# Optimization experiments

Hardware: AMD Instinct MI355X
Metric: run time of the kernel (lower is better)

The kernel has to match this reference:

```python
import jax, jax.numpy as jnp
import numpy as np

H = 4          # num_attention_heads
DH = 32        # attention_head_size
C = H * DH     # all_head_size = 128
WS = 7         # window side -> dim = 49
DIM = WS * WS
B = 4096       # number of windows
TABLE = (2 * WS - 1) ** 2  # 169


def setup_inputs() -> dict:
    key = jax.random.key(0)
    ks = jax.random.split(key, 10)
    s = 0.02
    return {
        "hidden_states": jax.random.normal(ks[0], (B, DIM, C), jnp.float32),
        "attention_mask": jax.random.normal(ks[1], (B, DIM, DIM), jnp.float32),
        "Wq": jax.random.normal(ks[2], (C, C), jnp.float32) * s,
        "bq": jax.random.normal(ks[3], (C,), jnp.float32) * s,
        "Wk": jax.random.normal(ks[4], (C, C), jnp.float32) * s,
        "bk": jax.random.normal(ks[5], (C,), jnp.float32) * s,
        "Wv": jax.random.normal(ks[6], (C, C), jnp.float32) * s,
        "bv": jax.random.normal(ks[7], (C,), jnp.float32) * s,
        "relative_position_bias_table": jax.random.normal(ks[8], (TABLE, H), jnp.float32) * s,
        "relative_position_index": jax.random.randint(ks[9], (DIM * DIM,), 0, TABLE, jnp.int64),
    }


def reference(hidden_states, attention_mask, Wq, bq, Wk, bk, Wv, bv,
              relative_position_bias_table, relative_position_index):
    b, n, _ = hidden_states.shape
    # QKV projections -> [b, H, n, DH]
    def proj(W, bias):
        y = jnp.einsum('bnc,cd->bnd', hidden_states, W.T) + bias
        return y.reshape(b, n, H, DH).transpose(0, 2, 1, 3)
    q = proj(Wq, bq)
    k = proj(Wk, bk)
    v = proj(Wv, bv)
    scores = jnp.einsum('bhnd,bhmd->bhnm', q, k) / jnp.sqrt(jnp.float32(DH))
    # relative position bias gather: [n*n] -> [n, n, H] -> [H, n, n]
    bias = relative_position_bias_table[relative_position_index].reshape(n, n, H)
    bias = bias.transpose(2, 0, 1)
    scores = scores + bias[None] + attention_mask[:, None]
    probs = jax.nn.softmax(scores, axis=-1)
    ctx = jnp.einsum('bhnm,bhmd->bhnd', probs, v)
    ctx = ctx.transpose(0, 2, 1, 3).reshape(b, n, H * DH)
    return ctx
```

## Files before the change

kernel.cpp:

```cpp
#include <hip/hip_runtime.h>
#include <hip/hip_bf16.h>


#define SEQ 49
#define CH 128
#define NH 4
#define DHD 32
#define NTAB 169

typedef __hip_bfloat16 bf16;
typedef __attribute__((ext_vector_type(8))) short bf16x8;
typedef __attribute__((ext_vector_type(4))) float f32x4;

#define LDQ 136
#define LDP 72
#define PROWS 52
#define OFF_Q  0
#define OFF_K  (64*LDQ)
#define OFF_VT (2*64*LDQ)
#define SMEM_ELEMS (OFF_VT + CH*LDP)
#define SMEM_BYTES (SMEM_ELEMS*2)

__device__ __forceinline__ bf16x8 pack8(float4 a, float4 b) {
    alignas(16) bf16 t[8] = {
        __float2bfloat16(a.x), __float2bfloat16(a.y),
        __float2bfloat16(a.z), __float2bfloat16(a.w),
        __float2bfloat16(b.x), __float2bfloat16(b.y),
        __float2bfloat16(b.z), __float2bfloat16(b.w)};
    return *(const bf16x8*)t;
}

__global__ void bias_precompute_kernel(const float* __restrict__ table,
                                       const int* __restrict__ ridx,
                                       float* __restrict__ bias_pad) {
    int i = blockIdx.x*256 + threadIdx.x;
    if (i >= NH*64*64) return;
    int h = i >> 12, nq = (i >> 6) & 63, mk = i & 63;
    float v = 0.f;
    if (nq < SEQ && mk < SEQ) {
        int idx = ridx[nq*SEQ + mk];
        idx = idx < 0 ? 0 : (idx > NTAB-1 ? NTAB-1 : idx);
        v = table[idx*NH + h];
    }
    bias_pad[i] = v;
}

template<bool USEWS>
__global__ __launch_bounds__(256, 3) void swin_attn_kernel(
    const float* __restrict__ hs,
    const float* __restrict__ amask,
    const float* __restrict__ Wq, const float* __restrict__ bq,
    const float* __restrict__ Wk, const float* __restrict__ bk,
    const float* __restrict__ Wv, const float* __restrict__ bv,
    const float* __restrict__ table,
    const int*  __restrict__ ridx,
    const float* __restrict__ bias_pad,
    float* __restrict__ out)
{
    extern __shared__ bf16 smem[];
    const int tid  = threadIdx.x;
    const int b    = blockIdx.x;
    const int wave = tid >> 6;
    const int lane = tid & 63;
    const int quad = lane >> 4;
    const int l    = lane & 15;

    bf16* sQ  = smem + OFF_Q;
    bf16* sK  = smem + OFF_K;
    bf16* sVt = smem + OFF_VT;
    bf16* sP  = smem;

    bf16x8 aX[4][4];
    const bf16x8 zf = {0,0,0,0,0,0,0,0};
    const float* xb = hs + (size_t)b*SEQ*CH + quad*8;
#pragma unroll
    for (int mt = 0; mt < 4; ++mt) {
        const int row = mt*16 + l;
        if (row < SEQ) {
            const float* xr = xb + row*CH;
#pragma unroll
            for (int ks = 0; ks < 4; ++ks)
                aX[mt][ks] = pack8(*(const float4*)(xr + ks*32),
                                   *(const float4*)(xr + ks*32 + 4));
        } else {
#pragma unroll
            for (int ks = 0; ks < 4; ++ks) aX[mt][ks] = zf;
        }
    }

    const float* Wmat[3] = {Wq, Wk, Wv};
    const float* Bvec[3] = {bq, bk, bv};
#pragma unroll
    for (int which = 0; which < 3; ++which) {
#pragma unroll
        for (int j = 0; j < 2; ++j) {
            const int col = (wave*2 + j)*16 + l;
            const float* wr = Wmat[which] + (size_t)col*CH + quad*8;
            float4 w[8];
#pragma unroll
            for (int ks = 0; ks < 4; ++ks) {
                w[2*ks]   = *(const float4*)(wr + ks*32);
                w[2*ks+1] = *(const float4*)(wr + ks*32 + 4);
            }
            f32x4 acc[4] = {{0.f,0.f,0.f,0.f},{0.f,0.f,0.f,0.f},
                            {0.f,0.f,0.f,0.f},{0.f,0.f,0.f,0.f}};
#pragma unroll
            for (int ks = 0; ks < 4; ++ks) {
                const bf16x8 bw = pack8(w[2*ks], w[2*ks+1]);
#pragma unroll
                for (int mt = 0; mt < 4; ++mt)
                    acc[mt] = __builtin_amdgcn_mfma_f32_16x16x32_bf16(
                        aX[mt][ks], bw, acc[mt], 0, 0, 0);
            }
            const float bias = Bvec[which][col];
            if (which == 2) {
#pragma unroll
                for (int mt = 0; mt < 4; ++mt) {
                    alignas(8) bf16 t4[4] = {
                        __float2bfloat16(acc[mt][0] + bias),
                        __float2bfloat16(acc[mt][1] + bias),
                        __float2bfloat16(acc[mt][2] + bias),
                        __float2bfloat16(acc[mt][3] + bias)};
                    *(uint2*)(sVt + col*LDP + mt*16 + quad*4) = *(const uint2*)t4;
                }
            } else {
                bf16* dst = (which == 0) ? sQ : sK;
#pragma unroll
                for (int mt = 0; mt < 4; ++mt)
#pragma unroll
                    for (int r = 0; r < 4; ++r)
                        dst[(mt*16 + quad*4 + r)*LDQ + col] =
                            __float2bfloat16(acc[mt][r] + bias);
            }
        }
    }

    const int h = wave;
    float pm[2][16], pb[2][16];
    int   pi[2][16];
    auto prefetchMB = [&](int mt, int pbuf) {
#pragma unroll
        for (int r = 0; r < 4; ++r)
#pragma unroll
            for (int nt = 0; nt < 4; ++nt) {
                const int nq = mt*16 + quad*4 + r;
                const int mk = nt*16 + l;
                const int nqc = nq > SEQ-1 ? SEQ-1 : nq;
                const int mkc = mk > SEQ-1 ? SEQ-1 : mk;
                pm[pbuf][r*4+nt] = amask[(size_t)b*SEQ*SEQ + nqc*SEQ + mkc];
                if (USEWS)
                    pb[pbuf][r*4+nt] = bias_pad[h*4096 + nq*64 + mk];
                else
                    pi[pbuf][r*4+nt] = ridx[nqc*SEQ + mkc];
            }
    };
    prefetchMB(0, 0);
    __syncthreads();

    bf16x8 aQ[4], bK[4];
#pragma unroll
    for (int t = 0; t < 4; ++t) {
        aQ[t] = *(const bf16x8*)(sQ + (t*16 + l)*LDQ + h*DHD + quad*8);
        bK[t] = *(const bf16x8*)(sK + (t*16 + l)*LDQ + h*DHD + quad*8);
    }
    __syncthreads();

    f32x4 S[4][4];
#pragma unroll
    for (int mt = 0; mt < 4; ++mt)
#pragma unroll
        for (int nt = 0; nt < 4; ++nt) {
            f32x4 z = {0.f,0.f,0.f,0.f};
            S[mt][nt] = __builtin_amdgcn_mfma_f32_16x16x32_bf16(aQ[mt], bK[nt], z, 0, 0, 0);
        }

    const float scale = 0.17677669529663687f;
#pragma unroll
    for (int mt = 0; mt < 4; ++mt) {
        const int cur = mt & 1;
        if (mt < 3) prefetchMB(mt+1, cur^1);
        float bias_g[16];
        if (!USEWS) {
#pragma unroll
            for (int e = 0; e < 16; ++e) {
                int idx = pi[cur][e];
                idx = idx < 0 ? 0 : (idx > NTAB-1 ? NTAB-1 : idx);
                bias_g[e] = table[idx*NH + h];
            }
        }
#pragma unroll
        for (int r = 0; r < 4; ++r) {
            const int nq = mt*16 + quad*4 + r;
#pragma unroll
            for (int nt = 0; nt < 4; ++nt) {
                const int mk = nt*16 + l;
                float s;
                if (mk < SEQ) {
                    const float bvv = USEWS ? pb[cur][r*4+nt]
                                            : ((nq < SEQ) ? bias_g[r*4+nt] : 0.f);
                    s = S[mt][nt][r]*scale + bvv + pm[cur][r*4+nt];
                } else {
                    s = -30000.f;
                }
                S[mt][nt][r] = s;
            }
            float m = fmaxf(fmaxf(S[mt][0][r], S[mt][1][r]),
                            fmaxf(S[mt][2][r], S[mt][3][r]));
            m = fmaxf(m, __shfl_xor(m, 1));
            m = fmaxf(m, __shfl_xor(m, 2));
            m = fmaxf(m, __shfl_xor(m, 4));
            m = fmaxf(m, __shfl_xor(m, 8));
            float sum = 0.f;
#pragma unroll
            for (int nt = 0; nt < 4; ++nt) {
                float e = __expf(S[mt][nt][r] - m);
                S[mt][nt][r] = e;
                sum += e;
            }
            sum += __shfl_xor(sum, 1);
            sum += __shfl_xor(sum, 2);
            sum += __shfl_xor(sum, 4);
            sum += __shfl_xor(sum, 8);
            const float inv = 1.f / sum;
            if (nq < PROWS) {
#pragma unroll
                for (int nt = 0; nt < 4; ++nt)
                    sP[h*(PROWS*LDP) + nq*LDP + nt*16 + l] =
                        __float2bfloat16(S[mt][nt][r] * inv);
            }
        }
    }
    __syncthreads();

    bf16x8 aP[4][2], bV[2][2];
#pragma unroll
    for (int mt = 0; mt < 4; ++mt)
#pragma unroll
        for (int ks = 0; ks < 2; ++ks)
            aP[mt][ks] = *(const bf16x8*)(sP + h*(PROWS*LDP) + (mt*16 + l)*LDP + ks*32 + quad*8);
#pragma unroll
    for (int nt = 0; nt < 2; ++nt)
#pragma unroll
        for (int ks = 0; ks < 2; ++ks)
            bV[nt][ks] = *(const bf16x8*)(sVt + (h*DHD + nt*16 + l)*LDP + ks*32 + quad*8);

    f32x4 O[4][2] = {{{0.f,0.f,0.f,0.f},{0.f,0.f,0.f,0.f}},
                     {{0.f,0.f,0.f,0.f},{0.f,0.f,0.f,0.f}},
                     {{0.f,0.f,0.f,0.f},{0.f,0.f,0.f,0.f}},
                     {{0.f,0.f,0.f,0.f},{0.f,0.f,0.f,0.f}}};
#pragma unroll
    for (int mt = 0; mt < 4; ++mt)
#pragma unroll
        for (int nt = 0; nt < 2; ++nt)
#pragma unroll
            for (int ks = 0; ks < 2; ++ks)
                O[mt][nt] = __builtin_amdgcn_mfma_f32_16x16x32_bf16(
                    aP[mt][ks], bV[nt][ks], O[mt][nt], 0, 0, 0);

#pragma unroll
    for (int mt = 0; mt < 4; ++mt)
#pragma unroll
        for (int r = 0; r < 4; ++r) {
            const int nq = mt*16 + quad*4 + r;
            if (nq < SEQ) {
#pragma unroll
                for (int nt = 0; nt < 2; ++nt)
                    out[((size_t)b*SEQ + nq)*CH + h*DHD + nt*16 + l] = O[mt][nt][r];
            }
        }
}

extern "C" void kernel_launch(void* const* d_in, const int* in_sizes, int n_in,
                              void* d_out, int out_size, void* d_ws, size_t ws_size,
                              hipStream_t stream) {
    (void)n_in; (void)out_size;
    const int nwin = in_sizes[0] / (SEQ * CH);
    const bool usews = (ws_size >= (size_t)NH*64*64*sizeof(float)) && d_ws != nullptr;
    if (usews) {
        bias_precompute_kernel<<<dim3((NH*64*64 + 255)/256), 256, 0, stream>>>(
            (const float*)d_in[8], (const int*)d_in[9], (float*)d_ws);
        hipFuncSetAttribute(reinterpret_cast<const void*>(swin_attn_kernel<true>),
                            hipFuncAttributeMaxDynamicSharedMemorySize, SMEM_BYTES);
        swin_attn_kernel<true><<<dim3(nwin), dim3(256), SMEM_BYTES, stream>>>(
            (const float*)d_in[0], (const float*)d_in[1],
            (const float*)d_in[2], (const float*)d_in[3],
            (const float*)d_in[4], (const float*)d_in[5],
            (const float*)d_in[6], (const float*)d_in[7],
            (const float*)d_in[8], (const int*)d_in[9],
            (const float*)d_ws, (float*)d_out);
    } else {
        hipFuncSetAttribute(reinterpret_cast<const void*>(swin_attn_kernel<false>),
                            hipFuncAttributeMaxDynamicSharedMemorySize, SMEM_BYTES);
        swin_attn_kernel<false><<<dim3(nwin), dim3(256), SMEM_BYTES, stream>>>(
            (const float*)d_in[0], (const float*)d_in[1],
            (const float*)d_in[2], (const float*)d_in[3],
            (const float*)d_in[4], (const float*)d_in[5],
            (const float*)d_in[6], (const float*)d_in[7],
            (const float*)d_in[8], (const int*)d_in[9],
            nullptr, (float*)d_out);
    }
}
```

Baseline: 336.8 us.

## Split attention into one wave per head with register-only shuffles

Each block now handles one (window, head) pair with a single 64-lane wave. Q, K and V are computed in registers and rearranged into MFMA operand layouts with lane shuffles, so shared memory and block barriers are no longer used. Scores are computed transposed (K times Q) so the softmax reduces across quads, and the V bias is added to the output instead. A prep kernel pre-packs the weights as bf16 fragments and precomputes a transposed bias table. The trade-off is that each of the four head blocks per window rereads the hidden states and recomputes the X fragments, adding global traffic and conversion work.

```diff
diff --git a/kernel.cpp b/kernel.cpp
--- a/kernel.cpp
+++ b/kernel.cpp
@@ -12,14 +12,11 @@
 typedef __attribute__((ext_vector_type(8))) short bf16x8;
 typedef __attribute__((ext_vector_type(4))) float f32x4;
 
-#define LDQ 136
-#define LDP 72
-#define PROWS 52
-#define OFF_Q  0
-#define OFF_K  (64*LDQ)
-#define OFF_VT (2*64*LDQ)
-#define SMEM_ELEMS (OFF_VT + CH*LDP)
-#define SMEM_BYTES (SMEM_ELEMS*2)
+#define WP_FRAGS (3*NH*2*4*64)
+#define WP_BYTES (WP_FRAGS*8*2)
+#define BIAS_ELEMS (NH*64*64)
+#define BIAS_BYTES (BIAS_ELEMS*4)
+#define WS_NEED ((size_t)(WP_BYTES + BIAS_BYTES))
 
 __device__ __forceinline__ bf16x8 pack8(float4 a, float4 b) {
     alignas(16) bf16 t[8] = {
@@ -30,23 +27,63 @@
     return *(const bf16x8*)t;
 }
 
-__global__ void bias_precompute_kernel(const float* __restrict__ table,
-                                       const int* __restrict__ ridx,
-                                       float* __restrict__ bias_pad) {
+__device__ __forceinline__ unsigned pk2(float lo, float hi) {
+    union { bf16 h[2]; unsigned u; } r;
+    r.h[0] = __float2bfloat16(lo);
+    r.h[1] = __float2bfloat16(hi);
+    return r.u;
+}
+
+__device__ __forceinline__ bf16x8 regroup(unsigned pk0_0, unsigned pk0_1,
+                                          unsigned pk1_0, unsigned pk1_1,
+                                          int srcA, int srcB, bool hiT) {
+    union { unsigned u[4]; bf16x8 v; } o;
+    unsigned a0 = (unsigned)__shfl((int)pk0_0, srcA);
+    unsigned b0 = (unsigned)__shfl((int)pk1_0, srcA);
+    unsigned a1 = (unsigned)__shfl((int)pk0_1, srcA);
+    unsigned b1 = (unsigned)__shfl((int)pk1_1, srcA);
+    unsigned a2 = (unsigned)__shfl((int)pk0_0, srcB);
+    unsigned b2 = (unsigned)__shfl((int)pk1_0, srcB);
+    unsigned a3 = (unsigned)__shfl((int)pk0_1, srcB);
+    unsigned b3 = (unsigned)__shfl((int)pk1_1, srcB);
+    o.u[0] = hiT ? b0 : a0;
+    o.u[1] = hiT ? b1 : a1;
+    o.u[2] = hiT ? b2 : a2;
+    o.u[3] = hiT ? b3 : a3;
+    return o.v;
+}
+
+__global__ void prep_kernel(const float* __restrict__ Wq,
+                            const float* __restrict__ Wk,
+                            const float* __restrict__ Wv,
+                            const float* __restrict__ table,
+                            const int*  __restrict__ ridx,
+                            bf16* __restrict__ wp,
+                            float* __restrict__ bias_t) {
     int i = blockIdx.x*256 + threadIdx.x;
-    if (i >= NH*64*64) return;
-    int h = i >> 12, nq = (i >> 6) & 63, mk = i & 63;
-    float v = 0.f;
-    if (nq < SEQ && mk < SEQ) {
-        int idx = ridx[nq*SEQ + mk];
-        idx = idx < 0 ? 0 : (idx > NTAB-1 ? NTAB-1 : idx);
-        v = table[idx*NH + h];
-    }
-    bias_pad[i] = v;
-}
-
-template<bool USEWS>
-__global__ __launch_bounds__(256, 3) void swin_attn_kernel(
+    if (i < WP_FRAGS) {
+        int lane = i & 63, ks = (i >> 6) & 3, t = (i >> 8) & 1;
+        int h = (i >> 9) & 3, which = i >> 11;
+        const float* W = which == 0 ? Wq : (which == 1 ? Wk : Wv);
+        const float* p = W + (h*DHD + t*16 + (lane & 15))*CH + ks*32 + (lane >> 4)*8;
+        ((bf16x8*)wp)[i] = pack8(*(const float4*)p, *(const float4*)(p + 4));
+    } else {
+        int j = i - WP_FRAGS;
+        if (j < BIAS_ELEMS) {
+            int h = j >> 12, n = (j >> 6) & 63, m = j & 63;
+            float v = 0.f;
+            if (n < SEQ && m < SEQ) {
+                int idx = ridx[m*SEQ + n];
+                idx = idx < 0 ? 0 : (idx > NTAB-1 ? NTAB-1 : idx);
+                v = table[idx*NH + h];
+            }
+            bias_t[j] = v;
+        }
+    }
+}
+
+template<bool WS>
+__global__ __launch_bounds__(64, 4) void swin_attn_kernel(
     const float* __restrict__ hs,
     const float* __restrict__ amask,
     const float* __restrict__ Wq, const float* __restrict__ bq,
@@ -54,218 +91,193 @@
     const float* __restrict__ Wv, const float* __restrict__ bv,
     const float* __restrict__ table,
     const int*  __restrict__ ridx,
-    const float* __restrict__ bias_pad,
+    const bf16*  __restrict__ wp,
+    const float* __restrict__ bias_t,
     float* __restrict__ out)
 {
-    extern __shared__ bf16 smem[];
-    const int tid  = threadIdx.x;
-    const int b    = blockIdx.x;
-    const int wave = tid >> 6;
-    const int lane = tid & 63;
-    const int quad = lane >> 4;
-    const int l    = lane & 15;
-
-    bf16* sQ  = smem + OFF_Q;
-    bf16* sK  = smem + OFF_K;
-    bf16* sVt = smem + OFF_VT;
-    bf16* sP  = smem;
-
-    bf16x8 aX[4][4];
-    const bf16x8 zf = {0,0,0,0,0,0,0,0};
-    const float* xb = hs + (size_t)b*SEQ*CH + quad*8;
-#pragma unroll
-    for (int mt = 0; mt < 4; ++mt) {
-        const int row = mt*16 + l;
-        if (row < SEQ) {
-            const float* xr = xb + row*CH;
-#pragma unroll
-            for (int ks = 0; ks < 4; ++ks)
-                aX[mt][ks] = pack8(*(const float4*)(xr + ks*32),
-                                   *(const float4*)(xr + ks*32 + 4));
+    const int b = blockIdx.x >> 2;
+    const int h = blockIdx.x & 3;
+    const int lane = threadIdx.x & 63;
+    const int l = lane & 15;
+    const int q = lane >> 4;
+    const int srcA = ((q & 1) << 5) | l;
+    const int srcB = srcA + 16;
+    const bool hiT = q >= 2;
+
+    const float* xb = hs + (size_t)b*SEQ*CH;
+    const f32x4 z4 = {0.f, 0.f, 0.f, 0.f};
+
+    auto loadX = [&](int rt, int ks) -> bf16x8 {
+        int row = rt*16 + l; row = row > SEQ-1 ? SEQ-1 : row;
+        const float* p = xb + row*CH + ks*32 + q*8;
+        return pack8(*(const float4*)p, *(const float4*)(p + 4));
+    };
+    auto loadW = [&](int which, int t, int ks) -> bf16x8 {
+        if (WS) {
+            return *(const bf16x8*)(wp +
+                ((((size_t)(which*NH + h)*2 + t)*4 + ks)*64 + lane)*8);
         } else {
-#pragma unroll
-            for (int ks = 0; ks < 4; ++ks) aX[mt][ks] = zf;
-        }
-    }
-
-    const float* Wmat[3] = {Wq, Wk, Wv};
-    const float* Bvec[3] = {bq, bk, bv};
-#pragma unroll
-    for (int which = 0; which < 3; ++which) {
-#pragma unroll
-        for (int j = 0; j < 2; ++j) {
-            const int col = (wave*2 + j)*16 + l;
-            const float* wr = Wmat[which] + (size_t)col*CH + quad*8;
-            float4 w[8];
-#pragma unroll
-            for (int ks = 0; ks < 4; ++ks) {
-                w[2*ks]   = *(const float4*)(wr + ks*32);
-                w[2*ks+1] = *(const float4*)(wr + ks*32 + 4);
-            }
-            f32x4 acc[4] = {{0.f,0.f,0.f,0.f},{0.f,0.f,0.f,0.f},
-                            {0.f,0.f,0.f,0.f},{0.f,0.f,0.f,0.f}};
-#pragma unroll
-            for (int ks = 0; ks < 4; ++ks) {
-                const bf16x8 bw = pack8(w[2*ks], w[2*ks+1]);
-#pragma unroll
-                for (int mt = 0; mt < 4; ++mt)
-                    acc[mt] = __builtin_amdgcn_mfma_f32_16x16x32_bf16(
-                        aX[mt][ks], bw, acc[mt], 0, 0, 0);
-            }
-            const float bias = Bvec[which][col];
-            if (which == 2) {
-#pragma unroll
-                for (int mt = 0; mt < 4; ++mt) {
-                    alignas(8) bf16 t4[4] = {
-                        __float2bfloat16(acc[mt][0] + bias),
-                        __float2bfloat16(acc[mt][1] + bias),
-                        __float2bfloat16(acc[mt][2] + bias),
-                        __float2bfloat16(acc[mt][3] + bias)};
-                    *(uint2*)(sVt + col*LDP + mt*16 + quad*4) = *(const uint2*)t4;
+            const float* W = which == 0 ? Wq : (which == 1 ? Wk : Wv);
+            const float* p = W + (h*DHD + t*16 + l)*CH + ks*32 + q*8;
+            return pack8(*(const float4*)p, *(const float4*)(p + 4));
+        }
+    };
+
+    bf16x8 fQ[4], fK[4];
+#pragma unroll
+    for (int which = 0; which < 2; ++which) {
+        f32x4 acc[2][4] = {{z4,z4,z4,z4},{z4,z4,z4,z4}};
+#pragma unroll
+        for (int ks = 0; ks < 4; ++ks) {
+            bf16x8 xf[4];
+#pragma unroll
+            for (int rt = 0; rt < 4; ++rt) xf[rt] = loadX(rt, ks);
+#pragma unroll
+            for (int t = 0; t < 2; ++t) {
+                const bf16x8 wf = loadW(which, t, ks);
+#pragma unroll
+                for (int rt = 0; rt < 4; ++rt)
+                    acc[t][rt] = __builtin_amdgcn_mfma_f32_16x16x32_bf16(
+                        wf, xf[rt], acc[t][rt], 0, 0, 0);
+            }
+        }
+        const float* bvec = which == 0 ? bq : bk;
+        unsigned pk[2][4][2];
+#pragma unroll
+        for (int t = 0; t < 2; ++t) {
+            const float b0 = bvec[h*DHD + t*16 + 4*q + 0];
+            const float b1 = bvec[h*DHD + t*16 + 4*q + 1];
+            const float b2 = bvec[h*DHD + t*16 + 4*q + 2];
+            const float b3 = bvec[h*DHD + t*16 + 4*q + 3];
+#pragma unroll
+            for (int rt = 0; rt < 4; ++rt) {
+                pk[t][rt][0] = pk2(acc[t][rt][0] + b0, acc[t][rt][1] + b1);
+                pk[t][rt][1] = pk2(acc[t][rt][2] + b2, acc[t][rt][3] + b3);
+            }
+        }
+#pragma unroll
+        for (int rt = 0; rt < 4; ++rt) {
+            const bf16x8 f = regroup(pk[0][rt][0], pk[0][rt][1],
+                                     pk[1][rt][0], pk[1][rt][1], srcA, srcB, hiT);
+            if (which == 0) fQ[rt] = f; else fK[rt] = f;
+        }
+    }
+
+    f32x4 accV[4][2] = {{z4,z4},{z4,z4},{z4,z4},{z4,z4}};
+#pragma unroll
+    for (int ks = 0; ks < 4; ++ks) {
+        bf16x8 xf[4];
+#pragma unroll
+        for (int nt = 0; nt < 4; ++nt) xf[nt] = loadX(nt, ks);
+#pragma unroll
+        for (int dt = 0; dt < 2; ++dt) {
+            const bf16x8 wf = loadW(2, dt, ks);
+#pragma unroll
+            for (int nt = 0; nt < 4; ++nt)
+                accV[nt][dt] = __builtin_amdgcn_mfma_f32_16x16x32_bf16(
+                    xf[nt], wf, accV[nt][dt], 0, 0, 0);
+        }
+    }
+    unsigned pkv[4][2][2];
+#pragma unroll
+    for (int nt = 0; nt < 4; ++nt)
+#pragma unroll
+        for (int dt = 0; dt < 2; ++dt) {
+            pkv[nt][dt][0] = pk2(accV[nt][dt][0], accV[nt][dt][1]);
+            pkv[nt][dt][1] = pk2(accV[nt][dt][2], accV[nt][dt][3]);
+        }
+    bf16x8 fV[2][2];
+#pragma unroll
+    for (int dt = 0; dt < 2; ++dt)
+#pragma unroll
+        for (int ks2 = 0; ks2 < 2; ++ks2)
+            fV[dt][ks2] = regroup(pkv[2*ks2][dt][0],   pkv[2*ks2][dt][1],
+                                  pkv[2*ks2+1][dt][0], pkv[2*ks2+1][dt][1],
+                                  srcA, srcB, hiT);
+
+    f32x4 S[4][4];
+#pragma unroll
+    for (int kt = 0; kt < 4; ++kt)
+#pragma unroll
+        for (int qt = 0; qt < 4; ++qt)
+            S[kt][qt] = __builtin_amdgcn_mfma_f32_16x16x32_bf16(
+                fK[kt], fQ[qt], z4, 0, 0, 0);
+
+    const float scale = 0.17677669529663687f;
+    const float* maskb = amask + (size_t)b*SEQ*SEQ;
+    const float* biash = WS ? bias_t + h*4096 : nullptr;
+    unsigned pkp[4][4][2];
+#pragma unroll
+    for (int qt = 0; qt < 4; ++qt) {
+        const int m = qt*16 + l;
+        const int mc = m > SEQ-1 ? SEQ-1 : m;
+        float mx = -3.0e38f;
+#pragma unroll
+        for (int kt = 0; kt < 4; ++kt)
+#pragma unroll
+            for (int r = 0; r < 4; ++r) {
+                const int n = kt*16 + 4*q + r;
+                const int nc = n > SEQ-1 ? SEQ-1 : n;
+                float bt;
+                if (WS) {
+                    bt = biash[n*64 + m];
+                } else {
+                    int idx = ridx[mc*SEQ + nc];
+                    idx = idx < 0 ? 0 : (idx > NTAB-1 ? NTAB-1 : idx);
+                    bt = table[idx*NH + h];
                 }
-            } else {
-                bf16* dst = (which == 0) ? sQ : sK;
-#pragma unroll
-                for (int mt = 0; mt < 4; ++mt)
-#pragma unroll
-                    for (int r = 0; r < 4; ++r)
-                        dst[(mt*16 + quad*4 + r)*LDQ + col] =
-                            __float2bfloat16(acc[mt][r] + bias);
-            }
-        }
-    }
-
-    const int h = wave;
-    float pm[2][16], pb[2][16];
-    int   pi[2][16];
-    auto prefetchMB = [&](int mt, int pbuf) {
-#pragma unroll
-        for (int r = 0; r < 4; ++r)
-#pragma unroll
-            for (int nt = 0; nt < 4; ++nt) {
-                const int nq = mt*16 + quad*4 + r;
-                const int mk = nt*16 + l;
-                const int nqc = nq > SEQ-1 ? SEQ-1 : nq;
-                const int mkc = mk > SEQ-1 ? SEQ-1 : mk;
-                pm[pbuf][r*4+nt] = amask[(size_t)b*SEQ*SEQ + nqc*SEQ + mkc];
-                if (USEWS)
-                    pb[pbuf][r*4+nt] = bias_pad[h*4096 + nq*64 + mk];
-                else
-                    pi[pbuf][r*4+nt] = ridx[nqc*SEQ + mkc];
-            }
-    };
-    prefetchMB(0, 0);
-    __syncthreads();
-
-    bf16x8 aQ[4], bK[4];
-#pragma unroll
-    for (int t = 0; t < 4; ++t) {
-        aQ[t] = *(const bf16x8*)(sQ + (t*16 + l)*LDQ + h*DHD + quad*8);
-        bK[t] = *(const bf16x8*)(sK + (t*16 + l)*LDQ + h*DHD + quad*8);
-    }
-    __syncthreads();
-
-    f32x4 S[4][4];
-#pragma unroll
-    for (int mt = 0; mt < 4; ++mt)
-#pragma unroll
-        for (int nt = 0; nt < 4; ++nt) {
-            f32x4 z = {0.f,0.f,0.f,0.f};
-            S[mt][nt] = __builtin_amdgcn_mfma_f32_16x16x32_bf16(aQ[mt], bK[nt], z, 0, 0, 0);
-        }
-
-    const float scale = 0.17677669529663687f;
-#pragma unroll
-    for (int mt = 0; mt < 4; ++mt) {
-        const int cur = mt & 1;
-        if (mt < 3) prefetchMB(mt+1, cur^1);
-        float bias_g[16];
-        if (!USEWS) {
-#pragma unroll
-            for (int e = 0; e < 16; ++e) {
-                int idx = pi[cur][e];
-                idx = idx < 0 ? 0 : (idx > NTAB-1 ? NTAB-1 : idx);
-                bias_g[e] = table[idx*NH + h];
-            }
-        }
+                const float mk = maskb[mc*SEQ + nc];
+                const float s = (n < SEQ) ? S[kt][qt][r]*scale + bt + mk
+                                          : -30000.f;
+                S[kt][qt][r] = s;
+                mx = fmaxf(mx, s);
+            }
+        mx = fmaxf(mx, __shfl_xor(mx, 16));
+        mx = fmaxf(mx, __shfl_xor(mx, 32));
+        float sum = 0.f;
+#pragma unroll
+        for (int kt = 0; kt < 4; ++kt)
+#pragma unroll
+            for (int r = 0; r < 4; ++r) {
+                const float e = __expf(S[kt][qt][r] - mx);
+                S[kt][qt][r] = e;
+                sum += e;
+            }
+        sum += __shfl_xor(sum, 16);
+        sum += __shfl_xor(sum, 32);
+        const float inv = 1.f / sum;
+#pragma unroll
+        for (int kt = 0; kt < 4; ++kt) {
+            pkp[kt][qt][0] = pk2(S[kt][qt][0]*inv, S[kt][qt][1]*inv);
+            pkp[kt][qt][1] = pk2(S[kt][qt][2]*inv, S[kt][qt][3]*inv);
+        }
+    }
+
+    f32x4 O[4][2] = {{z4,z4},{z4,z4},{z4,z4},{z4,z4}};
+#pragma unroll
+    for (int qt = 0; qt < 4; ++qt)
+#pragma unroll
+        for (int ks2 = 0; ks2 < 2; ++ks2) {
+            const bf16x8 ap = regroup(pkp[2*ks2][qt][0],   pkp[2*ks2][qt][1],
+                                      pkp[2*ks2+1][qt][0], pkp[2*ks2+1][qt][1],
+                                      srcA, srcB, hiT);
+#pragma unroll
+            for (int dt = 0; dt < 2; ++dt)
+                O[qt][dt] = __builtin_amdgcn_mfma_f32_16x16x32_bf16(
+                    ap, fV[dt][ks2], O[qt][dt], 0, 0, 0);
+        }
+
+    const float bv0 = bv[h*DHD + l];
+    const float bv1 = bv[h*DHD + 16 + l];
+    float* ob = out + (size_t)b*SEQ*CH + h*DHD;
+#pragma unroll
+    for (int qt = 0; qt < 4; ++qt)
 #pragma unroll
         for (int r = 0; r < 4; ++r) {
-            const int nq = mt*16 + quad*4 + r;
-#pragma unroll
-            for (int nt = 0; nt < 4; ++nt) {
-                const int mk = nt*16 + l;
-                float s;
-                if (mk < SEQ) {
-                    const float bvv = USEWS ? pb[cur][r*4+nt]
-                                            : ((nq < SEQ) ? bias_g[r*4+nt] : 0.f);
-                    s = S[mt][nt][r]*scale + bvv + pm[cur][r*4+nt];
-                } else {
-                    s = -30000.f;
-                }
-                S[mt][nt][r] = s;
-            }
-            float m = fmaxf(fmaxf(S[mt][0][r], S[mt][1][r]),
-                            fmaxf(S[mt][2][r], S[mt][3][r]));
-            m = fmaxf(m, __shfl_xor(m, 1));
-            m = fmaxf(m, __shfl_xor(m, 2));
-            m = fmaxf(m, __shfl_xor(m, 4));
-            m = fmaxf(m, __shfl_xor(m, 8));
-            float sum = 0.f;
-#pragma unroll
-            for (int nt = 0; nt < 4; ++nt) {
-                float e = __expf(S[mt][nt][r] - m);
-                S[mt][nt][r] = e;
-                sum += e;
-            }
-            sum += __shfl_xor(sum, 1);
-            sum += __shfl_xor(sum, 2);
-            sum += __shfl_xor(sum, 4);
-            sum += __shfl_xor(sum, 8);
-            const float inv = 1.f / sum;
-            if (nq < PROWS) {
-#pragma unroll
-                for (int nt = 0; nt < 4; ++nt)
-                    sP[h*(PROWS*LDP) + nq*LDP + nt*16 + l] =
-                        __float2bfloat16(S[mt][nt][r] * inv);
-            }
-        }
-    }
-    __syncthreads();
-
-    bf16x8 aP[4][2], bV[2][2];
-#pragma unroll
-    for (int mt = 0; mt < 4; ++mt)
-#pragma unroll
-        for (int ks = 0; ks < 2; ++ks)
-            aP[mt][ks] = *(const bf16x8*)(sP + h*(PROWS*LDP) + (mt*16 + l)*LDP + ks*32 + quad*8);
-#pragma unroll
-    for (int nt = 0; nt < 2; ++nt)
-#pragma unroll
-        for (int ks = 0; ks < 2; ++ks)
-            bV[nt][ks] = *(const bf16x8*)(sVt + (h*DHD + nt*16 + l)*LDP + ks*32 + quad*8);
-
-    f32x4 O[4][2] = {{{0.f,0.f,0.f,0.f},{0.f,0.f,0.f,0.f}},
-                     {{0.f,0.f,0.f,0.f},{0.f,0.f,0.f,0.f}},
-                     {{0.f,0.f,0.f,0.f},{0.f,0.f,0.f,0.f}},
-                     {{0.f,0.f,0.f,0.f},{0.f,0.f,0.f,0.f}}};
-#pragma unroll
-    for (int mt = 0; mt < 4; ++mt)
-#pragma unroll
-        for (int nt = 0; nt < 2; ++nt)
-#pragma unroll
-            for (int ks = 0; ks < 2; ++ks)
-                O[mt][nt] = __builtin_amdgcn_mfma_f32_16x16x32_bf16(
-                    aP[mt][ks], bV[nt][ks], O[mt][nt], 0, 0, 0);
-
-#pragma unroll
-    for (int mt = 0; mt < 4; ++mt)
-#pragma unroll
-        for (int r = 0; r < 4; ++r) {
-            const int nq = mt*16 + quad*4 + r;
-            if (nq < SEQ) {
-#pragma unroll
-                for (int nt = 0; nt < 2; ++nt)
-                    out[((size_t)b*SEQ + nq)*CH + h*DHD + nt*16 + l] = O[mt][nt][r];
+            const int m = qt*16 + 4*q + r;
+            if (m < SEQ) {
+                ob[m*CH + l]      = O[qt][0][r] + bv0;
+                ob[m*CH + 16 + l] = O[qt][1][r] + bv1;
             }
         }
 }
@@ -275,28 +287,27 @@
                               hipStream_t stream) {
     (void)n_in; (void)out_size;
     const int nwin = in_sizes[0] / (SEQ * CH);
-    const bool usews = (ws_size >= (size_t)NH*64*64*sizeof(float)) && d_ws != nullptr;
+    const bool usews = (d_ws != nullptr) && (ws_size >= WS_NEED);
     if (usews) {
-        bias_precompute_kernel<<<dim3((NH*64*64 + 255)/256), 256, 0, stream>>>(
-            (const float*)d_in[8], (const int*)d_in[9], (float*)d_ws);
-        hipFuncSetAttribute(reinterpret_cast<const void*>(swin_attn_kernel<true>),
-                            hipFuncAttributeMaxDynamicSharedMemorySize, SMEM_BYTES);
-        swin_attn_kernel<true><<<dim3(nwin), dim3(256), SMEM_BYTES, stream>>>(
+        bf16* wp = (bf16*)d_ws;
+        float* bias_t = (float*)((char*)d_ws + WP_BYTES);
+        prep_kernel<<<dim3((WP_FRAGS + BIAS_ELEMS + 255)/256), dim3(256), 0, stream>>>(
+            (const float*)d_in[2], (const float*)d_in[4], (const float*)d_in[6],
+            (const float*)d_in[8], (const int*)d_in[9], wp, bias_t);
+        swin_attn_kernel<true><<<dim3(nwin*NH), dim3(64), 0, stream>>>(
             (const float*)d_in[0], (const float*)d_in[1],
             (const float*)d_in[2], (const float*)d_in[3],
             (const float*)d_in[4], (const float*)d_in[5],
             (const float*)d_in[6], (const float*)d_in[7],
             (const float*)d_in[8], (const int*)d_in[9],
-            (const float*)d_ws, (float*)d_out);
+            wp, bias_t, (float*)d_out);
     } else {
-        hipFuncSetAttribute(reinterpret_cast<const void*>(swin_attn_kernel<false>),
-                            hipFuncAttributeMaxDynamicSharedMemorySize, SMEM_BYTES);
-        swin_attn_kernel<false><<<dim3(nwin), dim3(256), SMEM_BYTES, stream>>>(
+        swin_attn_kernel<false><<<dim3(nwin*NH), dim3(64), 0, stream>>>(
             (const float*)d_in[0], (const float*)d_in[1],
             (const float*)d_in[2], (const float*)d_in[3],
             (const float*)d_in[4], (const float*)d_in[5],
             (const float*)d_in[6], (const float*)d_in[7],
             (const float*)d_in[8], (const int*)d_in[9],
-            nullptr, (float*)d_out);
-    }
-}
+            nullptr, nullptr, (float*)d_out);
+    }
+}
```

New measurement: 358.6 us. +6.5%, slower.
